# Kernel optimization log

Hardware: AMD Instinct MI355X
Metric: run time of the kernel (lower is better)

Reference implementation:

```python
import jax, jax.numpy as jnp
import numpy as np

N_HEADS = 4
NUM_GROUPS = 32
EPS = 1e-6


def _nin(t, W, b):
    # 1x1 conv as dense over channel dim: [B,C,H,W] x [C,D] -> [B,D,H,W]
    return jnp.einsum('bchw,cd->bdhw', t, W) + b[None, :, None, None]


def setup_inputs() -> dict:
    key = jax.random.key(0)
    ks = jax.random.split(key, 12)
    B, C, H, W = 8, 256, 32, 32
    Tc = 512
    Cin = C + Tc  # 768
    x = jax.random.normal(ks[0], (B, C, H, W), dtype=jnp.float32)
    text_feat = jax.random.normal(ks[1], (B, Tc), dtype=jnp.float32)
    gn_gamma = jnp.ones((Cin,), dtype=jnp.float32)
    gn_beta = jnp.zeros((Cin,), dtype=jnp.float32)
    scale = 1.0 / np.sqrt(Cin)
    W0 = jax.random.normal(ks[2], (Cin, C), dtype=jnp.float32) * scale
    b0 = jnp.zeros((C,), dtype=jnp.float32)
    W1 = jax.random.normal(ks[3], (Cin, C), dtype=jnp.float32) * scale
    b1 = jnp.zeros((C,), dtype=jnp.float32)
    W2 = jax.random.normal(ks[4], (Cin, C), dtype=jnp.float32) * scale
    b2 = jnp.zeros((C,), dtype=jnp.float32)
    return {"x": x, "text_feat": text_feat, "gn_gamma": gn_gamma, "gn_beta": gn_beta,
            "W0": W0, "b0": b0, "W1": W1, "b1": b1, "W2": W2, "b2": b2}


def reference(x, text_feat, gn_gamma, gn_beta, W0, b0, W1, b1, W2, b2):
    B, C, H, W = x.shape
    # broadcast text features spatially and concat on channel dim
    tf = jnp.broadcast_to(text_feat[:, :, None, None], (B, text_feat.shape[1], H, W))
    h = jnp.concatenate([x, tf], axis=1)  # [B, C+Tc, H, W]
    Ctot = h.shape[1]
    # GroupNorm(32, Ctot), eps=1e-6
    hg = h.reshape(B, NUM_GROUPS, Ctot // NUM_GROUPS, H, W)
    mu = hg.mean(axis=(2, 3, 4), keepdims=True)
    var = hg.var(axis=(2, 3, 4), keepdims=True)
    hn = ((hg - mu) * jax.lax.rsqrt(var + EPS)).reshape(B, Ctot, H, W)
    hn = hn * gn_gamma[None, :, None, None] + gn_beta[None, :, None, None]
    q = _nin(hn, W0, b0)
    k = _nin(hn, W1, b1)
    v = _nin(hn, W2, b2)
    Ch = C // N_HEADS
    qh = q.reshape(B * N_HEADS, Ch, H, W)
    kh = k.reshape(B * N_HEADS, Ch, H, W)
    vh = v.reshape(B * N_HEADS, Ch, H, W)
    # full HW x HW attention scores, softmax over flattened key positions
    w = jnp.einsum('bchw,bcij->bhwij', qh, kh) * (Ch ** -0.5)
    w = jax.nn.softmax(w.reshape(B * N_HEADS, H, W, H * W), axis=-1)
    w = w.reshape(B * N_HEADS, H, W, H, W)
    ho = jnp.einsum('bhwij,bcij->bchw', w, vh).reshape(B, C, H, W)
    return x + ho
```

## Files before the change

kernel.cpp:

```cpp
#include <hip/hip_runtime.h>
#include <math.h>

#define BATCH 8
#define CX 256
#define TC 512
#define CIN 768
#define HW_TOT 1024
#define NH 4
#define CHD 64

typedef __attribute__((ext_vector_type(8))) short short8;
typedef __attribute__((ext_vector_type(4))) short s4v;
typedef __attribute__((ext_vector_type(4))) float floatx4;
typedef __attribute__((ext_vector_type(4))) int int4v;

#define QSCALE 0.18033688f

static __device__ __forceinline__ short f2bf(float f) {
    union { float f; unsigned u; } c; c.f = f;
    unsigned r = (c.u + 0x7fffu + ((c.u >> 16) & 1u)) >> 16;
    return (short)r;
}

static __device__ __forceinline__ int pack_trunc(float lo, float hi) {
    union { float f; unsigned u; } L, H;
    L.f = lo; H.f = hi;
    return (int)((H.u & 0xffff0000u) | (L.u >> 16));
}

__global__ __launch_bounds__(256)
void gn_kernel(const float* __restrict__ x, const float* __restrict__ tf,
               const float* __restrict__ gamma, const float* __restrict__ beta,
               float* __restrict__ scale, float* __restrict__ shift,
               float* __restrict__ tc) {
    const int b = blockIdx.x >> 5;
    const int g = blockIdx.x & 31;
    const int t = threadIdx.x;
    const int w = t >> 6, lane = t & 63;
    if (blockIdx.x < 24) tc[blockIdx.x * 256 + t] = 0.f;

    float s = 0.f, ss = 0.f;
    #pragma unroll
    for (int rr = 0; rr < 6; rr++) {
        const int row = w * 6 + rr;
        const int cg = g * 24 + row;
        if (cg < CX) {
            const float4* p = (const float4*)(x + ((size_t)b * CX + cg) * HW_TOT);
            #pragma unroll
            for (int i = 0; i < 4; i++) {
                float4 v = p[lane + 64 * i];
                s += v.x + v.y + v.z + v.w;
                ss += v.x * v.x + v.y * v.y + v.z * v.z + v.w * v.w;
            }
        } else {
            float v = tf[b * TC + cg - CX];
            s += 16.f * v;
            ss += 16.f * v * v;
        }
    }
    #pragma unroll
    for (int d = 1; d < 64; d <<= 1) {
        s += __shfl_xor(s, d);
        ss += __shfl_xor(ss, d);
    }
    __shared__ float rs_[4], rss_[4];
    if (lane == 0) { rs_[w] = s; rss_[w] = ss; }
    __syncthreads();
    const float S  = rs_[0] + rs_[1] + rs_[2] + rs_[3];
    const float SS = rss_[0] + rss_[1] + rss_[2] + rss_[3];
    const float inv_n = 1.f / (24 * 1024);
    const float mean = S * inv_n;
    const float var = SS * inv_n - mean * mean;
    const float r = rsqrtf(var + 1e-6f);
    if (t < 24) {
        int cg = g * 24 + t;
        float sc = gamma[cg] * r;
        scale[b * CIN + cg] = sc;
        shift[b * CIN + cg] = beta[cg] - mean * sc;
    }
}

__global__ __launch_bounds__(256)
void prep_kernel(const float* __restrict__ x, const float* __restrict__ tf,
                 const float* __restrict__ scale, const float* __restrict__ shift,
                 const float* __restrict__ W0, const float* __restrict__ W1,
                 const float* __restrict__ W2,
                 short* __restrict__ hnT, short* __restrict__ Wt,
                 float* __restrict__ tc) {
    __shared__ float hs[128];
    __shared__ float red[4][64];
    const int bx = blockIdx.x;
    const int t = threadIdx.x;
    if (bx < 256) {
        int id = (bx & 31) * 256 + t;
        int b = id >> 10;
        const float* xb = x + (size_t)b * CX * HW_TOT + (id & 1023);
        const float* scb = scale + b * CIN;
        const float* shb = shift + b * CIN;
        short* outp = hnT + (size_t)id * CX;
        int c0base = (bx >> 5) * 32;
        for (int c0 = c0base; c0 < c0base + 32; c0 += 8) {
            short8 o;
            #pragma unroll
            for (int i = 0; i < 8; i++) {
                float v = xb[(size_t)(c0 + i) * HW_TOT];
                o[i] = f2bf(v * scb[c0 + i] + shb[c0 + i]);
            }
            *(short8*)(outp + c0) = o;
        }
    } else if (bx < 268) {
        int m = bx - 256;
        int dg = (m % 3) * 256 + t;
        int which = dg >> 8, d = dg & 255;
        const float* Wm = (which == 0) ? W0 : (which == 1) ? W1 : W2;
        int c0base = (m / 3) * 64;
        for (int c0 = c0base; c0 < c0base + 64; c0 += 8) {
            short8 o;
            #pragma unroll
            for (int i = 0; i < 8; i++) o[i] = f2bf(Wm[(size_t)(c0 + i) * CX + d]);
            *(short8*)(Wt + (size_t)dg * CX + c0) = o;
        }
    } else {
        int m = bx - 268;
        int ks = m & 3;
        int b = (m >> 2) & 7, dt = m >> 5;
        int which = dt >> 2, d0 = (dt & 3) * 64;
        const float* Wm = (which == 0) ? W0 : (which == 1) ? W1 : W2;
        if (t < 128) {
            int c = ks * 128 + t;
            hs[t] = tf[b * TC + c] * scale[b * CIN + CX + c] + shift[b * CIN + CX + c];
        }
        __syncthreads();
        int td = t & 63, tq = t >> 6;
        float acc = 0.f;
        const float* wp = Wm + (size_t)(CX + ks * 128 + tq * 32) * CX + d0 + td;
        #pragma unroll 8
        for (int c = 0; c < 32; c++)
            acc = fmaf(hs[tq * 32 + c], wp[(size_t)c * CX], acc);
        red[tq][td] = acc;
        __syncthreads();
        if (t < 64)
            atomicAdd(&tc[b * CIN + which * CX + d0 + t],
                      red[0][t] + red[1][t] + red[2][t] + red[3][t]);
    }
}

__global__ __launch_bounds__(256)
void qkv_gemm(const short* __restrict__ hnT, const short* __restrict__ Wt,
              const float* __restrict__ tc,
              const float* __restrict__ b0, const float* __restrict__ b1,
              const float* __restrict__ b2,
              short* __restrict__ qb, short* __restrict__ kb, short* __restrict__ vb) {
    const int hw0 = blockIdx.x * 64, dt = blockIdx.y, b = blockIdx.z;
    const int which = dt >> 2;
    const int col0 = (dt & 3) * 64;
    const int dg0 = which * 256 + col0;
    const bool OV = (which == 2);

    __shared__ short At[64 * 72];
    __shared__ short Bt[64 * 72];

    const int t = threadIdx.x;
    const int w = t >> 6, l = t & 63;
    const int wm = w >> 1, wn = w & 1;
    const int l15 = l & 15, q = l >> 4;
    const int srow = t >> 2, sch = (t & 3) * 16;

    const short* gA = hnT + (size_t)(b * HW_TOT + hw0 + srow) * CX + sch;
    const short* gB = Wt + (size_t)(dg0 + srow) * CX + sch;

    floatx4 acc[2][2] = {};
    for (int k0 = 0; k0 < CX; k0 += 64) {
        __syncthreads();
        *(short8*)(At + srow * 72 + sch)     = *(const short8*)(gA + k0);
        *(short8*)(At + srow * 72 + sch + 8) = *(const short8*)(gA + k0 + 8);
        *(short8*)(Bt + srow * 72 + sch)     = *(const short8*)(gB + k0);
        *(short8*)(Bt + srow * 72 + sch + 8) = *(const short8*)(gB + k0 + 8);
        __syncthreads();
        const short* aB = OV ? Bt : At;
        const short* bB = OV ? At : Bt;
        #pragma unroll
        for (int kc = 0; kc < 2; kc++) {
            short8 af[2], bf2[2];
            #pragma unroll
            for (int mt = 0; mt < 2; mt++)
                af[mt] = *(const short8*)(aB + (wm * 32 + mt * 16 + l15) * 72 + kc * 32 + q * 8);
            #pragma unroll
            for (int nt = 0; nt < 2; nt++)
                bf2[nt] = *(const short8*)(bB + (wn * 32 + nt * 16 + l15) * 72 + kc * 32 + q * 8);
            #pragma unroll
            for (int mt = 0; mt < 2; mt++)
                #pragma unroll
                for (int nt = 0; nt < 2; nt++)
                    acc[mt][nt] = __builtin_amdgcn_mfma_f32_16x16x32_bf16(
                        af[mt], bf2[nt], acc[mt][nt], 0, 0, 0);
        }
    }

    __syncthreads();
    const float* bias = (which == 0) ? b0 : (which == 1) ? b1 : b2;
    if (!OV) {
        const float qs = (which == 0) ? QSCALE : 1.0f;
        float cadd[2];
        #pragma unroll
        for (int nt = 0; nt < 2; nt++) {
            int d = col0 + wn * 32 + nt * 16 + l15;
            cadd[nt] = bias[d] + tc[b * CIN + which * CX + d];
        }
        #pragma unroll
        for (int mt = 0; mt < 2; mt++)
            #pragma unroll
            for (int rr = 0; rr < 4; rr++)
                #pragma unroll
                for (int nt = 0; nt < 2; nt++)
                    At[(wm * 32 + mt * 16 + q * 4 + rr) * 72 + wn * 32 + nt * 16 + l15]
                        = f2bf((acc[mt][nt][rr] + cadd[nt]) * qs);
    } else {
        #pragma unroll
        for (int mt = 0; mt < 2; mt++)
            #pragma unroll
            for (int rr = 0; rr < 4; rr++) {
                int d = col0 + wm * 32 + mt * 16 + q * 4 + rr;
                float radd = bias[d] + tc[b * CIN + 2 * CX + d];
                #pragma unroll
                for (int nt = 0; nt < 2; nt++)
                    At[(wm * 32 + mt * 16 + q * 4 + rr) * 72 + wn * 32 + nt * 16 + l15]
                        = f2bf(acc[mt][nt][rr] + radd);
            }
    }
    __syncthreads();
    short8 v0 = *(const short8*)(At + srow * 72 + sch);
    short8 v1 = *(const short8*)(At + srow * 72 + sch + 8);
    if (!OV) {
        short* outp = (which == 0) ? qb : kb;
        size_t off = (size_t)(b * HW_TOT + hw0 + srow) * CX + col0 + sch;
        *(short8*)(outp + off) = v0;
        *(short8*)(outp + off + 8) = v1;
    } else {
        size_t off = (size_t)(b * CX + col0 + srow) * HW_TOT + hw0 + sch;
        *(short8*)(vb + off) = v0;
        *(short8*)(vb + off + 8) = v1;
    }
}

__global__ __launch_bounds__(256)
void attn_kernel(const short* __restrict__ qb, const short* __restrict__ kb,
                 const short* __restrict__ vb, const float* __restrict__ x,
                 float* __restrict__ out) {
    const int qt = blockIdx.x, bh = blockIdx.y;
    const int b = bh >> 2, h = bh & 3;
    const int hw0 = qt * 64;

    __shared__ short Qs[64 * 72];
    __shared__ short Ks[2][64 * 72];
    __shared__ short Vs[2][64 * 72];

    const int t = threadIdx.x;
    const int w = t >> 6, l = t & 63;
    const int l15 = l & 15, q = l >> 4;
    const int srow = t >> 2, sch = (t & 3) * 16;
    const int vpos0 = ((sch >> 5) << 5) + ((sch >> 4) & 1) * 4;

    {
        const short* gq = qb + (size_t)(b * HW_TOT + hw0 + srow) * CX + h * CHD + sch;
        *(short8*)(Qs + srow * 72 + sch)     = *(const short8*)gq;
        *(short8*)(Qs + srow * 72 + sch + 8) = *(const short8*)(gq + 8);
    }

    short8 pk0, pk1, pv0, pv1;
    {
        const short* gk = kb + (size_t)(b * HW_TOT + 0 + srow) * CX + h * CHD + sch;
        pk0 = *(const short8*)gk;
        pk1 = *(const short8*)(gk + 8);
        const short* gv = vb + (size_t)(b * CX + h * CHD + srow) * HW_TOT + 0 + sch;
        pv0 = *(const short8*)gv;
        pv1 = *(const short8*)(gv + 8);
        *(short8*)(Ks[0] + srow * 72 + sch)     = pk0;
        *(short8*)(Ks[0] + srow * 72 + sch + 8) = pk1;
        short* vrow = Vs[0] + srow * 72 + vpos0;
        *(s4v*)(vrow)      = __builtin_shufflevector(pv0, pv0, 0, 1, 2, 3);
        *(s4v*)(vrow + 8)  = __builtin_shufflevector(pv0, pv0, 4, 5, 6, 7);
        *(s4v*)(vrow + 16) = __builtin_shufflevector(pv1, pv1, 0, 1, 2, 3);
        *(s4v*)(vrow + 24) = __builtin_shufflevector(pv1, pv1, 4, 5, 6, 7);
    }
    __syncthreads();
    const short8 aq0 = *(const short8*)(Qs + (w * 16 + l15) * 72 + q * 8);
    const short8 aq1 = *(const short8*)(Qs + (w * 16 + l15) * 72 + 32 + q * 8);

    union { int4v i; short8 s; } ones;
    ones.i[0] = 0x3f803f80; ones.i[1] = 0x3f803f80;
    ones.i[2] = 0x3f803f80; ones.i[3] = 0x3f803f80;

    floatx4 oacc[4] = {};
    floatx4 lacc = {};

    for (int jj = 0; jj < 16; jj++) {
        const int cur = jj & 1;
        if (jj < 15) {
            const int j0 = (jj + 1) * 64;
            const short* gk = kb + (size_t)(b * HW_TOT + j0 + srow) * CX + h * CHD + sch;
            pk0 = *(const short8*)gk;
            pk1 = *(const short8*)(gk + 8);
            const short* gv = vb + (size_t)(b * CX + h * CHD + srow) * HW_TOT + j0 + sch;
            pv0 = *(const short8*)gv;
            pv1 = *(const short8*)(gv + 8);
        }

        const short* Kc = Ks[cur];
        floatx4 sacc[4] = {};
        #pragma unroll
        for (int nt = 0; nt < 4; nt++) {
            short8 kf0 = *(const short8*)(Kc + (nt * 16 + l15) * 72 + q * 8);
            short8 kf1 = *(const short8*)(Kc + (nt * 16 + l15) * 72 + 32 + q * 8);
            sacc[nt] = __builtin_amdgcn_mfma_f32_16x16x32_bf16(kf0, aq0, sacc[nt], 0, 0, 0);
            sacc[nt] = __builtin_amdgcn_mfma_f32_16x16x32_bf16(kf1, aq1, sacc[nt], 0, 0, 0);
        }

        union { int4v i; short8 s; } u0, u1;
        #pragma unroll
        for (int nt = 0; nt < 4; nt++) {
            float e0 = exp2f(sacc[nt][0]);
            float e1 = exp2f(sacc[nt][1]);
            float e2 = exp2f(sacc[nt][2]);
            float e3 = exp2f(sacc[nt][3]);
            if (nt < 2) {
                u0.i[nt * 2]     = pack_trunc(e0, e1);
                u0.i[nt * 2 + 1] = pack_trunc(e2, e3);
            } else {
                u1.i[(nt - 2) * 2]     = pack_trunc(e0, e1);
                u1.i[(nt - 2) * 2 + 1] = pack_trunc(e2, e3);
            }
        }

        lacc = __builtin_amdgcn_mfma_f32_16x16x32_bf16(ones.s, u0.s, lacc, 0, 0, 0);
        lacc = __builtin_amdgcn_mfma_f32_16x16x32_bf16(ones.s, u1.s, lacc, 0, 0, 0);

        const short* Vc = Vs[cur];
        #pragma unroll
        for (int ct = 0; ct < 4; ct++) {
            const short* vr = Vc + (ct * 16 + l15) * 72;
            #pragma unroll
            for (int kcc = 0; kcc < 2; kcc++) {
                short8 vf = *(const short8*)(vr + kcc * 32 + q * 8);
                oacc[ct] = __builtin_amdgcn_mfma_f32_16x16x32_bf16(
                    vf, kcc ? u1.s : u0.s, oacc[ct], 0, 0, 0);
            }
        }

        if (jj < 15) {
            *(short8*)(Ks[1 - cur] + srow * 72 + sch)     = pk0;
            *(short8*)(Ks[1 - cur] + srow * 72 + sch + 8) = pk1;
            short* vrow = Vs[1 - cur] + srow * 72 + vpos0;
            *(s4v*)(vrow)      = __builtin_shufflevector(pv0, pv0, 0, 1, 2, 3);
            *(s4v*)(vrow + 8)  = __builtin_shufflevector(pv0, pv0, 4, 5, 6, 7);
            *(s4v*)(vrow + 16) = __builtin_shufflevector(pv1, pv1, 0, 1, 2, 3);
            *(s4v*)(vrow + 24) = __builtin_shufflevector(pv1, pv1, 4, 5, 6, 7);
            __syncthreads();
        }
    }

    const float rinv = 1.f / lacc[0];
    #pragma unroll
    for (int ct = 0; ct < 4; ct++)
        #pragma unroll
        for (int r = 0; r < 4; r++) {
            int c = h * CHD + ct * 16 + q * 4 + r;
            size_t idx = (size_t)(b * CX + c) * HW_TOT + hw0 + w * 16 + l15;
            out[idx] = x[idx] + oacc[ct][r] * rinv;
        }
}

extern "C" void kernel_launch(void* const* d_in, const int* in_sizes, int n_in,
                              void* d_out, int out_size, void* d_ws, size_t ws_size,
                              hipStream_t stream) {
    (void)in_sizes; (void)n_in; (void)out_size; (void)ws_size;
    const float* x     = (const float*)d_in[0];
    const float* tf    = (const float*)d_in[1];
    const float* gamma = (const float*)d_in[2];
    const float* beta  = (const float*)d_in[3];
    const float* W0 = (const float*)d_in[4];
    const float* b0 = (const float*)d_in[5];
    const float* W1 = (const float*)d_in[6];
    const float* b1 = (const float*)d_in[7];
    const float* W2 = (const float*)d_in[8];
    const float* b2 = (const float*)d_in[9];

    char* ws = (char*)d_ws;
    float* scale  = (float*)(ws);
    float* shift  = (float*)(ws + 24576);
    float* tcb    = (float*)(ws + 49152);
    short* Wt     = (short*)(ws + 73728);
    short* hnT    = (short*)(ws + 466944);
    short* qb     = (short*)(ws + 4661248);
    short* kb     = (short*)(ws + 8855552);
    short* vb     = (short*)(ws + 13049856);

    hipLaunchKernelGGL(gn_kernel, dim3(256), dim3(256), 0, stream,
                       x, tf, gamma, beta, scale, shift, tcb);
    hipLaunchKernelGGL(prep_kernel, dim3(652), dim3(256), 0, stream,
                       x, tf, scale, shift, W0, W1, W2, hnT, Wt, tcb);
    hipLaunchKernelGGL(qkv_gemm, dim3(16, 12, BATCH), dim3(256), 0, stream,
                       hnT, Wt, tcb, b0, b1, b2, qb, kb, vb);
    hipLaunchKernelGGL(attn_kernel, dim3(16, 32), dim3(256), 0, stream,
                       qb, kb, vb, x, (float*)d_out);
}
```

Baseline: 119.0 us.

## Process 128 query rows per attention block to reuse K/V tiles

Each attention workgroup now handles 128 query positions instead of 64, with every wave computing two 16-row groups against the same K and V fragments loaded from shared memory. This halves global K/V traffic and LDS fragment reads per query, and halves the grid to 256 blocks. It also adds a barrier before overwriting the double buffer, fixing a potential race. The costs are higher register pressure from doubled accumulators and fewer blocks, which may lower occupancy on a 256-CU device.

```diff
diff --git a/kernel.cpp b/kernel.cpp
--- a/kernel.cpp
+++ b/kernel.cpp
@@ -249,9 +249,9 @@
                  float* __restrict__ out) {
     const int qt = blockIdx.x, bh = blockIdx.y;
     const int b = bh >> 2, h = bh & 3;
-    const int hw0 = qt * 64;
-
-    __shared__ short Qs[64 * 72];
+    const int hw0 = qt * 128;
+
+    __shared__ short Qs[128 * 72];
     __shared__ short Ks[2][64 * 72];
     __shared__ short Vs[2][64 * 72];
 
@@ -262,9 +262,13 @@
     const int vpos0 = ((sch >> 5) << 5) + ((sch >> 4) & 1) * 4;
 
     {
-        const short* gq = qb + (size_t)(b * HW_TOT + hw0 + srow) * CX + h * CHD + sch;
-        *(short8*)(Qs + srow * 72 + sch)     = *(const short8*)gq;
-        *(short8*)(Qs + srow * 72 + sch + 8) = *(const short8*)(gq + 8);
+        #pragma unroll
+        for (int rr = 0; rr < 2; rr++) {
+            const short* gq = qb + (size_t)(b * HW_TOT + hw0 + rr * 64 + srow) * CX
+                            + h * CHD + sch;
+            *(short8*)(Qs + (rr * 64 + srow) * 72 + sch)     = *(const short8*)gq;
+            *(short8*)(Qs + (rr * 64 + srow) * 72 + sch + 8) = *(const short8*)(gq + 8);
+        }
     }
 
     short8 pk0, pk1, pv0, pv1;
@@ -284,15 +288,20 @@
         *(s4v*)(vrow + 24) = __builtin_shufflevector(pv1, pv1, 4, 5, 6, 7);
     }
     __syncthreads();
-    const short8 aq0 = *(const short8*)(Qs + (w * 16 + l15) * 72 + q * 8);
-    const short8 aq1 = *(const short8*)(Qs + (w * 16 + l15) * 72 + 32 + q * 8);
+
+    short8 aq[2][2];
+    #pragma unroll
+    for (int g = 0; g < 2; g++) {
+        aq[g][0] = *(const short8*)(Qs + (w * 32 + g * 16 + l15) * 72 + q * 8);
+        aq[g][1] = *(const short8*)(Qs + (w * 32 + g * 16 + l15) * 72 + 32 + q * 8);
+    }
 
     union { int4v i; short8 s; } ones;
     ones.i[0] = 0x3f803f80; ones.i[1] = 0x3f803f80;
     ones.i[2] = 0x3f803f80; ones.i[3] = 0x3f803f80;
 
-    floatx4 oacc[4] = {};
-    floatx4 lacc = {};
+    floatx4 oacc[2][4] = {};
+    floatx4 lacc[2] = {};
 
     for (int jj = 0; jj < 16; jj++) {
         const int cur = jj & 1;
@@ -307,33 +316,36 @@
         }
 
         const short* Kc = Ks[cur];
-        floatx4 sacc[4] = {};
+        floatx4 sacc[2][4] = {};
         #pragma unroll
         for (int nt = 0; nt < 4; nt++) {
             short8 kf0 = *(const short8*)(Kc + (nt * 16 + l15) * 72 + q * 8);
             short8 kf1 = *(const short8*)(Kc + (nt * 16 + l15) * 72 + 32 + q * 8);
-            sacc[nt] = __builtin_amdgcn_mfma_f32_16x16x32_bf16(kf0, aq0, sacc[nt], 0, 0, 0);
-            sacc[nt] = __builtin_amdgcn_mfma_f32_16x16x32_bf16(kf1, aq1, sacc[nt], 0, 0, 0);
-        }
-
-        union { int4v i; short8 s; } u0, u1;
-        #pragma unroll
-        for (int nt = 0; nt < 4; nt++) {
-            float e0 = exp2f(sacc[nt][0]);
-            float e1 = exp2f(sacc[nt][1]);
-            float e2 = exp2f(sacc[nt][2]);
-            float e3 = exp2f(sacc[nt][3]);
-            if (nt < 2) {
-                u0.i[nt * 2]     = pack_trunc(e0, e1);
-                u0.i[nt * 2 + 1] = pack_trunc(e2, e3);
-            } else {
-                u1.i[(nt - 2) * 2]     = pack_trunc(e0, e1);
-                u1.i[(nt - 2) * 2 + 1] = pack_trunc(e2, e3);
-            }
-        }
-
-        lacc = __builtin_amdgcn_mfma_f32_16x16x32_bf16(ones.s, u0.s, lacc, 0, 0, 0);
-        lacc = __builtin_amdgcn_mfma_f32_16x16x32_bf16(ones.s, u1.s, lacc, 0, 0, 0);
+            #pragma unroll
+            for (int g = 0; g < 2; g++) {
+                sacc[g][nt] = __builtin_amdgcn_mfma_f32_16x16x32_bf16(kf0, aq[g][0], sacc[g][nt], 0, 0, 0);
+                sacc[g][nt] = __builtin_amdgcn_mfma_f32_16x16x32_bf16(kf1, aq[g][1], sacc[g][nt], 0, 0, 0);
+            }
+        }
+
+        union { int4v i; short8 s; } u[2][2];
+        #pragma unroll
+        for (int g = 0; g < 2; g++)
+            #pragma unroll
+            for (int nt = 0; nt < 4; nt++) {
+                float e0 = exp2f(sacc[g][nt][0]);
+                float e1 = exp2f(sacc[g][nt][1]);
+                float e2 = exp2f(sacc[g][nt][2]);
+                float e3 = exp2f(sacc[g][nt][3]);
+                u[g][nt >> 1].i[(nt & 1) * 2]     = pack_trunc(e0, e1);
+                u[g][nt >> 1].i[(nt & 1) * 2 + 1] = pack_trunc(e2, e3);
+            }
+
+        #pragma unroll
+        for (int g = 0; g < 2; g++) {
+            lacc[g] = __builtin_amdgcn_mfma_f32_16x16x32_bf16(ones.s, u[g][0].s, lacc[g], 0, 0, 0);
+            lacc[g] = __builtin_amdgcn_mfma_f32_16x16x32_bf16(ones.s, u[g][1].s, lacc[g], 0, 0, 0);
+        }
 
         const short* Vc = Vs[cur];
         #pragma unroll
@@ -342,12 +354,15 @@
             #pragma unroll
             for (int kcc = 0; kcc < 2; kcc++) {
                 short8 vf = *(const short8*)(vr + kcc * 32 + q * 8);
-                oacc[ct] = __builtin_amdgcn_mfma_f32_16x16x32_bf16(
-                    vf, kcc ? u1.s : u0.s, oacc[ct], 0, 0, 0);
+                #pragma unroll
+                for (int g = 0; g < 2; g++)
+                    oacc[g][ct] = __builtin_amdgcn_mfma_f32_16x16x32_bf16(
+                        vf, u[g][kcc].s, oacc[g][ct], 0, 0, 0);
             }
         }
 
         if (jj < 15) {
+            __syncthreads();
             *(short8*)(Ks[1 - cur] + srow * 72 + sch)     = pk0;
             *(short8*)(Ks[1 - cur] + srow * 72 + sch + 8) = pk1;
             short* vrow = Vs[1 - cur] + srow * 72 + vpos0;
@@ -359,15 +374,18 @@
         }
     }
 
-    const float rinv = 1.f / lacc[0];
     #pragma unroll
-    for (int ct = 0; ct < 4; ct++)
-        #pragma unroll
-        for (int r = 0; r < 4; r++) {
-            int c = h * CHD + ct * 16 + q * 4 + r;
-            size_t idx = (size_t)(b * CX + c) * HW_TOT + hw0 + w * 16 + l15;
-            out[idx] = x[idx] + oacc[ct][r] * rinv;
-        }
+    for (int g = 0; g < 2; g++) {
+        const float rinv = 1.f / lacc[g][0];
+        #pragma unroll
+        for (int ct = 0; ct < 4; ct++)
+            #pragma unroll
+            for (int r = 0; r < 4; r++) {
+                int c = h * CHD + ct * 16 + q * 4 + r;
+                size_t idx = (size_t)(b * CX + c) * HW_TOT + hw0 + w * 32 + g * 16 + l15;
+                out[idx] = x[idx] + oacc[g][ct][r] * rinv;
+            }
+    }
 }
 
 extern "C" void kernel_launch(void* const* d_in, const int* in_sizes, int n_in,
@@ -401,6 +419,6 @@
                        x, tf, scale, shift, W0, W1, W2, hnT, Wt, tcb);
     hipLaunchKernelGGL(qkv_gemm, dim3(16, 12, BATCH), dim3(256), 0, stream,
                        hnT, Wt, tcb, b0, b1, b2, qb, kb, vb);
-    hipLaunchKernelGGL(attn_kernel, dim3(16, 32), dim3(256), 0, stream,
+    hipLaunchKernelGGL(attn_kernel, dim3(8, 32), dim3(256), 0, stream,
                        qb, kb, vb, x, (float*)d_out);
 }
```

Result: slower. 124.9 us (+5.0%).
